# Optimization experiments

Measured on AMD Instinct MI355X. Metric: run time of the kernel, lower is better.

## Reference

```python
import jax, jax.numpy as jnp
import numpy as np

B, L, D = 4, 4096, 1024
S, H, DH = 256, 16, 64
TOPK = 8
NEG_INF = float('-inf')


def setup_inputs() -> dict:
    key = jax.random.key(0)
    ks = jax.random.split(key, 10)
    scale = 1.0 / np.sqrt(D)
    return {
        'token_states': jax.random.normal(ks[0], (B, L, D), dtype=jnp.float32),
        'Z_sets': jax.random.normal(ks[1], (B, S, H, DH), dtype=jnp.float32),
        'desc_q': jax.random.normal(ks[2], (B, S, D), dtype=jnp.float32),
        'mask_q': jnp.ones((B, S), dtype=bool),
        'Wg_w': jax.random.normal(ks[3], (D, D), dtype=jnp.float32) * scale,
        'Wg_b': jnp.zeros((D,), dtype=jnp.float32),
        'Wd_w': jax.random.normal(ks[4], (D, D), dtype=jnp.float32) * scale,
        'Wd_b': jnp.zeros((D,), dtype=jnp.float32),
        'out_w': jax.random.normal(ks[5], (D, D), dtype=jnp.float32) * scale,
        'out_b': jnp.zeros((D,), dtype=jnp.float32),
    }


def reference(token_states, Z_sets, desc_q, mask_q, Wg_w, Wg_b, Wd_w, Wd_b, out_w, out_b):
    # torch nn.Linear: y = x @ W.T + b
    Tproj = token_states @ Wg_w.T + Wg_b          # (B,L,D)
    Dproj = desc_q @ Wd_w.T + Wd_b                # (B,S,D)
    logits = jnp.einsum('bld,bsd->bls', Tproj, Dproj)  # (B,L,S)
    logits = jnp.where(mask_q[:, None, :], logits, NEG_INF)
    if TOPK > 0 and S > TOPK:
        vals, idx = jax.lax.top_k(logits, TOPK)   # (B,L,K)
        probs = jax.nn.softmax(vals, axis=-1)     # softmax over the K kept logits
        b_ix = jnp.arange(B)[:, None, None]
        l_ix = jnp.arange(L)[None, :, None]
        G = jnp.zeros_like(logits).at[b_ix, l_ix, idx].set(probs)
    else:
        G = jax.nn.softmax(logits, axis=-1)
    mix = jnp.einsum('bls,bshd->blhd', G, Z_sets)  # (B,L,H,DH)
    return mix.reshape(B, L, D) @ out_w.T + out_b
```

## Files before the change

### kernel.cpp

```cpp
#include <hip/hip_runtime.h>
#include <hip/hip_bf16.h>
#include <stdint.h>


#define B_ 4
#define L_ 4096
#define D_ 1024
#define S_ 256

typedef short s16x8 __attribute__((ext_vector_type(8)));
typedef float f32x4 __attribute__((ext_vector_type(4)));

__device__ __forceinline__ unsigned short f2bf(float f) {
  uint32_t u = __float_as_uint(f);
  u += 0x7FFFu + ((u >> 16) & 1u);
  return (unsigned short)(u >> 16);
}
__device__ __forceinline__ float bf2f(unsigned short h) {
  return __uint_as_float(((uint32_t)h) << 16);
}
__device__ __forceinline__ int kperm32(int k5) {
  return (((k5 >> 2) & 3) << 3) | (((k5 >> 4) & 1) << 2) | (k5 & 3);
}

__global__ __launch_bounds__(256)
void prep_all(const float* __restrict__ desc, const float* __restrict__ Zf,
              const float* __restrict__ Wd, const float* __restrict__ oW,
              const float* __restrict__ Wg,
              unsigned short* __restrict__ dHi, unsigned short* __restrict__ dLo,
              unsigned short* __restrict__ zHi,
              unsigned short* __restrict__ wdHi, unsigned short* __restrict__ wdLo,
              unsigned short* __restrict__ owHi,
              unsigned short* __restrict__ wgTHi, unsigned short* __restrict__ wgTLo) {
  __shared__ float t[64][65];
  const int bid = blockIdx.x, tid = threadIdx.x;
  if (bid < 4096) {
    const float* src[4] = {desc, Zf, Wd, oW};
    unsigned short* hi[4] = {dHi, zHi, wdHi, owHi};
    unsigned short* lo[4] = {dLo, nullptr, wdLo, nullptr};
    int job = bid >> 10;
    int i = (bid & 1023) * 256 + tid;
    float4 v = reinterpret_cast<const float4*>(src[job])[i];
    int idx = i << 2;
    int nidx = (idx & ~31) | (((idx >> 2) & 3) << 3) | (((idx >> 4) & 1) << 2);
    float a[4] = {v.x, v.y, v.z, v.w};
    unsigned short hb[4];
#pragma unroll
    for (int e = 0; e < 4; ++e) hb[e] = f2bf(a[e]);
    *reinterpret_cast<ushort4*>(hi[job] + nidx) = make_ushort4(hb[0], hb[1], hb[2], hb[3]);
    if (lo[job]) {
      unsigned short lb[4];
#pragma unroll
      for (int e = 0; e < 4; ++e) lb[e] = f2bf(a[e] - bf2f(hb[e]));
      *reinterpret_cast<ushort4*>(lo[job] + nidx) = make_ushort4(lb[0], lb[1], lb[2], lb[3]);
    }
  } else {
    int tb = bid - 4096;
    int bx = tb & 15, by = tb >> 4;
    int c = tid & 63, r0 = tid >> 6;
#pragma unroll
    for (int rr = 0; rr < 16; ++rr) {
      int r = r0 * 16 + rr;
      t[r][c] = Wg[(size_t)(by * 64 + r) * 1024 + bx * 64 + c];
    }
    __syncthreads();
#pragma unroll
    for (int rr = 0; rr < 16; ++rr) {
      int r = r0 * 16 + rr;
      float v = t[c][r];
      int kcol = by * 64 + (c & 32) + kperm32(c & 31);
      size_t o = (size_t)(bx * 64 + r) * 1024 + kcol;
      unsigned short hb = f2bf(v);
      wgTHi[o] = hb;
      wgTLo[o] = f2bf(v - bf2f(hb));
    }
  }
}

__global__ __launch_bounds__(256, 2)
void gemm_a(const unsigned short* __restrict__ dHi, const unsigned short* __restrict__ dLo,
            const unsigned short* __restrict__ wdHi, const unsigned short* __restrict__ wdLo,
            const unsigned short* __restrict__ zHi, const unsigned short* __restrict__ owHi,
            float* __restrict__ P) {
  __shared__ unsigned short lAh[128 * 64], lAl[128 * 64];
  __shared__ unsigned short lBh[128 * 64], lBl[128 * 64];
  const int tid = threadIdx.x;
  const int w = tid >> 6, l = tid & 63;
  const int g = l >> 4, r15 = l & 15;
  const int rowBase = blockIdx.y * 128, colBase = blockIdx.x * 128;
  const int prob = blockIdx.z >> 1, kz = blockIdx.z & 1;
  const bool t3 = (prob == 0);
  const unsigned short* Ah = t3 ? dHi : zHi;
  const unsigned short* Bh = t3 ? wdHi : owHi;
  const int wr = (w >> 1) * 64, wc = (w & 1) * 64;
  const int k0 = kz * 512;

  f32x4 acc[4][4] = {};

  for (int kt = k0; kt < k0 + 512; kt += 64) {
    __syncthreads();
#pragma unroll
    for (int j = 0; j < 4; ++j) {
      int cl = j * 256 + tid;
      int r = cl >> 3;
      int c16 = (cl & 7) ^ (r & 7);
      long ao = (long)(rowBase + r) * 1024 + kt + c16 * 8;
      long bo = (long)(colBase + r) * 1024 + kt + c16 * 8;
      size_t doff = (size_t)(j * 256 + w * 64) * 8;
      __builtin_amdgcn_global_load_lds((const __attribute__((address_space(1))) void*)(Ah + ao),
                                       (__attribute__((address_space(3))) void*)(lAh + doff), 16, 0, 0);
      __builtin_amdgcn_global_load_lds((const __attribute__((address_space(1))) void*)(Bh + bo),
                                       (__attribute__((address_space(3))) void*)(lBh + doff), 16, 0, 0);
      if (t3) {
        __builtin_amdgcn_global_load_lds((const __attribute__((address_space(1))) void*)(dLo + ao),
                                         (__attribute__((address_space(3))) void*)(lAl + doff), 16, 0, 0);
        __builtin_amdgcn_global_load_lds((const __attribute__((address_space(1))) void*)(wdLo + bo),
                                         (__attribute__((address_space(3))) void*)(lBl + doff), 16, 0, 0);
      }
    }
    __syncthreads();
#pragma unroll
    for (int ks = 0; ks < 2; ++ks) {
      s16x8 ah[4], bh[4];
#pragma unroll
      for (int m = 0; m < 4; ++m) {
        int row = wr + m * 16 + r15;
        int offb = (row * 128 + ks * 64 + g * 16) ^ ((row & 7) << 4);
        ah[m] = *reinterpret_cast<const s16x8*>(reinterpret_cast<const char*>(lAh) + offb);
      }
#pragma unroll
      for (int n = 0; n < 4; ++n) {
        int row = wc + n * 16 + r15;
        int offb = (row * 128 + ks * 64 + g * 16) ^ ((row & 7) << 4);
        bh[n] = *reinterpret_cast<const s16x8*>(reinterpret_cast<const char*>(lBh) + offb);
      }
#pragma unroll
      for (int m = 0; m < 4; ++m)
#pragma unroll
        for (int n = 0; n < 4; ++n)
          acc[m][n] = __builtin_amdgcn_mfma_f32_16x16x32_bf16(ah[m], bh[n], acc[m][n], 0, 0, 0);
      if (t3) {
        s16x8 al[4], bl[4];
#pragma unroll
        for (int m = 0; m < 4; ++m) {
          int row = wr + m * 16 + r15;
          int offb = (row * 128 + ks * 64 + g * 16) ^ ((row & 7) << 4);
          al[m] = *reinterpret_cast<const s16x8*>(reinterpret_cast<const char*>(lAl) + offb);
        }
#pragma unroll
        for (int n = 0; n < 4; ++n) {
          int row = wc + n * 16 + r15;
          int offb = (row * 128 + ks * 64 + g * 16) ^ ((row & 7) << 4);
          bl[n] = *reinterpret_cast<const s16x8*>(reinterpret_cast<const char*>(lBl) + offb);
        }
#pragma unroll
        for (int m = 0; m < 4; ++m)
#pragma unroll
          for (int n = 0; n < 4; ++n) {
            acc[m][n] = __builtin_amdgcn_mfma_f32_16x16x32_bf16(al[m], bh[n], acc[m][n], 0, 0, 0);
            acc[m][n] = __builtin_amdgcn_mfma_f32_16x16x32_bf16(ah[m], bl[n], acc[m][n], 0, 0, 0);
          }
      }
    }
  }

  float* Cz = P + (long)blockIdx.z * (1 << 20);
#pragma unroll
  for (int m = 0; m < 4; ++m)
#pragma unroll
    for (int n = 0; n < 4; ++n) {
      int col = colBase + wc + n * 16 + r15;
#pragma unroll
      for (int q = 0; q < 4; ++q) {
        int row = rowBase + wr + m * 16 + g * 4 + q;
        Cz[(long)row * 1024 + col] = acc[m][n][q];
      }
    }
}

template <int KSPLIT>
__global__ __launch_bounds__(256, 2)
void gemm_f3(const unsigned short* __restrict__ Ahi, const unsigned short* __restrict__ Alo,
             const unsigned short* __restrict__ Bhi, const unsigned short* __restrict__ Blo,
             float* __restrict__ C, int K, long partStride) {
  __shared__ unsigned short lAh[128 * 64], lAl[128 * 64];
  __shared__ unsigned short lBh[128 * 64], lBl[128 * 64];
  const int tid = threadIdx.x;
  const int w = tid >> 6, l = tid & 63;
  const int g = l >> 4, r15 = l & 15;
  const int rowBase = blockIdx.y * 128, colBase = blockIdx.x * 128;
  const int kz = blockIdx.z % KSPLIT;
  const int wr = (w >> 1) * 64, wc = (w & 1) * 64;
  const int chunk = K / KSPLIT, k0 = kz * chunk;

  f32x4 acc[4][4] = {};

  for (int kt = k0; kt < k0 + chunk; kt += 64) {
    __syncthreads();
#pragma unroll
    for (int j = 0; j < 4; ++j) {
      int cl = j * 256 + tid;
      int r = cl >> 3;
      int c16 = (cl & 7) ^ (r & 7);
      long ao = (long)(rowBase + r) * K + kt + c16 * 8;
      long bo = (long)(colBase + r) * K + kt + c16 * 8;
      size_t doff = (size_t)(j * 256 + w * 64) * 8;
      __builtin_amdgcn_global_load_lds((const __attribute__((address_space(1))) void*)(Ahi + ao),
                                       (__attribute__((address_space(3))) void*)(lAh + doff), 16, 0, 0);
      __builtin_amdgcn_global_load_lds((const __attribute__((address_space(1))) void*)(Alo + ao),
                                       (__attribute__((address_space(3))) void*)(lAl + doff), 16, 0, 0);
      __builtin_amdgcn_global_load_lds((const __attribute__((address_space(1))) void*)(Bhi + bo),
                                       (__attribute__((address_space(3))) void*)(lBh + doff), 16, 0, 0);
      __builtin_amdgcn_global_load_lds((const __attribute__((address_space(1))) void*)(Blo + bo),
                                       (__attribute__((address_space(3))) void*)(lBl + doff), 16, 0, 0);
    }
    __syncthreads();
#pragma unroll
    for (int ks = 0; ks < 2; ++ks) {
      s16x8 ah[4], al[4], bh[4], bl[4];
#pragma unroll
      for (int m = 0; m < 4; ++m) {
        int row = wr + m * 16 + r15;
        int offb = (row * 128 + ks * 64 + g * 16) ^ ((row & 7) << 4);
        ah[m] = *reinterpret_cast<const s16x8*>(reinterpret_cast<const char*>(lAh) + offb);
        al[m] = *reinterpret_cast<const s16x8*>(reinterpret_cast<const char*>(lAl) + offb);
      }
#pragma unroll
      for (int n = 0; n < 4; ++n) {
        int row = wc + n * 16 + r15;
        int offb = (row * 128 + ks * 64 + g * 16) ^ ((row & 7) << 4);
        bh[n] = *reinterpret_cast<const s16x8*>(reinterpret_cast<const char*>(lBh) + offb);
        bl[n] = *reinterpret_cast<const s16x8*>(reinterpret_cast<const char*>(lBl) + offb);
      }
#pragma unroll
      for (int m = 0; m < 4; ++m)
#pragma unroll
        for (int n = 0; n < 4; ++n) {
          acc[m][n] = __builtin_amdgcn_mfma_f32_16x16x32_bf16(ah[m], bh[n], acc[m][n], 0, 0, 0);
          acc[m][n] = __builtin_amdgcn_mfma_f32_16x16x32_bf16(al[m], bh[n], acc[m][n], 0, 0, 0);
          acc[m][n] = __builtin_amdgcn_mfma_f32_16x16x32_bf16(ah[m], bl[n], acc[m][n], 0, 0, 0);
        }
    }
  }

  float* Cz = C + (long)blockIdx.z * partStride;
#pragma unroll
  for (int m = 0; m < 4; ++m)
#pragma unroll
    for (int n = 0; n < 4; ++n) {
      int col = colBase + wc + n * 16 + r15;
#pragma unroll
      for (int q = 0; q < 4; ++q) {
        int row = rowBase + wr + m * 16 + g * 4 + q;
        Cz[(long)row * 1024 + col] = acc[m][n][q];
      }
    }
}

__global__ __launch_bounds__(256)
void post_a(const float* __restrict__ P, const float* __restrict__ Wd_b,
            const float* __restrict__ out_b, const float* __restrict__ Wg_b,
            unsigned short* __restrict__ dpHi, unsigned short* __restrict__ dpLo,
            unsigned short* __restrict__ zwB, float* __restrict__ cb) {
  int w = threadIdx.x >> 6, l = threadIdx.x & 63;
  int job = blockIdx.x;
  if (job < 256) {
    int row = job * 4 + w;
    const float* r0 = P + (size_t)row * 1024;
    const float* r1 = r0 + (1 << 20);
    float s = 0.f;
#pragma unroll
    for (int j = 0; j < 4; ++j) {
      int i = j * 64 + l;
      float4 a = reinterpret_cast<const float4*>(r0)[i];
      float4 b = reinterpret_cast<const float4*>(r1)[i];
      float4 bb = reinterpret_cast<const float4*>(Wd_b)[i & 255];
      float4 v = make_float4(a.x + b.x + bb.x, a.y + b.y + bb.y,
                             a.z + b.z + bb.z, a.w + b.w + bb.w);
      float4 g = reinterpret_cast<const float4*>(Wg_b)[i & 255];
      s += v.x * g.x + v.y * g.y + v.z * g.z + v.w * g.w;
      int idx = i << 2;
      int nidx = (idx & ~31) | (((idx >> 2) & 3) << 3) | (((idx >> 4) & 1) << 2);
      float arr[4] = {v.x, v.y, v.z, v.w};
      unsigned short hb[4], lb[4];
#pragma unroll
      for (int e = 0; e < 4; ++e) {
        hb[e] = f2bf(arr[e]);
        lb[e] = f2bf(arr[e] - bf2f(hb[e]));
      }
      *reinterpret_cast<ushort4*>(dpHi + (size_t)row * 1024 + nidx) =
          make_ushort4(hb[0], hb[1], hb[2], hb[3]);
      *reinterpret_cast<ushort4*>(dpLo + (size_t)row * 1024 + nidx) =
          make_ushort4(lb[0], lb[1], lb[2], lb[3]);
    }
#pragma unroll
    for (int off = 32; off; off >>= 1) s += __shfl_xor(s, off);
    if (l == 0) cb[row] = s;
  } else {
    int row = (job - 256) * 4 + w;
    const float* r0 = P + 2 * (1 << 20) + (size_t)row * 1024;
    const float* r1 = r0 + (1 << 20);
#pragma unroll
    for (int j = 0; j < 4; ++j) {
      int i = j * 64 + l;
      float4 a = reinterpret_cast<const float4*>(r0)[i];
      float4 b = reinterpret_cast<const float4*>(r1)[i];
      float4 bb = reinterpret_cast<const float4*>(out_b)[i & 255];
      *reinterpret_cast<ushort4*>(zwB + (size_t)row * 1024 + (i << 2)) =
          make_ushort4(f2bf(a.x + b.x + bb.x), f2bf(a.y + b.y + bb.y),
                       f2bf(a.z + b.z + bb.z), f2bf(a.w + b.w + bb.w));
    }
  }
}

__global__ __launch_bounds__(256)
void post_mt(const float* __restrict__ P, unsigned short* __restrict__ hi,
             unsigned short* __restrict__ lo) {
  int w = threadIdx.x >> 6, l = threadIdx.x & 63;
  int row = blockIdx.x * 4 + w;
  const float* r0 = P + (size_t)row * 1024;
#pragma unroll
  for (int j = 0; j < 4; ++j) {
    int i = j * 64 + l;
    float4 a = reinterpret_cast<const float4*>(r0)[i];
    float4 b = reinterpret_cast<const float4*>(r0 + (1 << 20))[i];
    float4 c = reinterpret_cast<const float4*>(r0 + 2 * (1 << 20))[i];
    float4 d = reinterpret_cast<const float4*>(r0 + 3 * (1 << 20))[i];
    float arr[4] = {a.x + b.x + c.x + d.x, a.y + b.y + c.y + d.y,
                    a.z + b.z + c.z + d.z, a.w + b.w + c.w + d.w};
    int idx = i << 2;
    int nidx = (idx & ~31) | (((idx >> 2) & 3) << 3) | (((idx >> 4) & 1) << 2);
    unsigned short hb[4], lb[4];
#pragma unroll
    for (int e = 0; e < 4; ++e) {
      hb[e] = f2bf(arr[e]);
      lb[e] = f2bf(arr[e] - bf2f(hb[e]));
    }
    *reinterpret_cast<ushort4*>(hi + (size_t)row * 1024 + nidx) =
        make_ushort4(hb[0], hb[1], hb[2], hb[3]);
    *reinterpret_cast<ushort4*>(lo + (size_t)row * 1024 + nidx) =
        make_ushort4(lb[0], lb[1], lb[2], lb[3]);
  }
}

template <int KSPLIT>
__global__ __launch_bounds__(256, 2)
void gemm_af32(const float* __restrict__ A,
               const unsigned short* __restrict__ Bhi, const unsigned short* __restrict__ Blo,
               float* __restrict__ Ct, int K,
               long batchA, long batchB, long batchCt, long kzStrideCt) {
  __shared__ unsigned short lAh[128 * 64], lAl[128 * 64];
  __shared__ unsigned short lBh[128 * 64], lBl[128 * 64];
  const int tid = threadIdx.x;
  const int w = tid >> 6, l = tid & 63;
  const int g = l >> 4, r15 = l & 15;
  const int nwg = gridDim.x * gridDim.y * gridDim.z;
  int h = blockIdx.x + gridDim.x * (blockIdx.y + gridDim.y * blockIdx.z);
  int lg = (h % 8) * (nwg / 8) + h / 8;
  const int bx = lg % gridDim.x;
  const int by = (lg / gridDim.x) % gridDim.y;
  const int bzz = lg / (gridDim.x * gridDim.y);
  const int rowBase = by * 128, colBase = bx * 128;
  const int bz = bzz / KSPLIT, kz = bzz % KSPLIT;
  const long zA = (long)bz * batchA, zB = (long)bz * batchB;
  const int wr = (w >> 1) * 64, wc = (w & 1) * 64;
  const int chunk = K / KSPLIT, k0 = kz * chunk;

  f32x4 acc[4][4] = {};

  for (int kt = k0; kt < k0 + chunk; kt += 64) {
    float4 av[8];
#pragma unroll
    for (int j = 0; j < 8; ++j) {
      int cl = j * 256 + tid;
      int r = cl >> 4, k4 = cl & 15;
      av[j] = *reinterpret_cast<const float4*>(A + zA + (long)(rowBase + r) * K + kt + k4 * 4);
    }
    __syncthreads();
#pragma unroll
    for (int j = 0; j < 4; ++j) {
      int cl = j * 256 + tid;
      int r = cl >> 3;
      int c16 = (cl & 7) ^ (r & 7);
      long bo = zB + (long)(colBase + r) * K + kt + c16 * 8;
      size_t doff = (size_t)(j * 256 + w * 64) * 8;
      __builtin_amdgcn_global_load_lds((const __attribute__((address_space(1))) void*)(Bhi + bo),
                                       (__attribute__((address_space(3))) void*)(lBh + doff), 16, 0, 0);
      __builtin_amdgcn_global_load_lds((const __attribute__((address_space(1))) void*)(Blo + bo),
                                       (__attribute__((address_space(3))) void*)(lBl + doff), 16, 0, 0);
    }
#pragma unroll
    for (int j = 0; j < 8; ++j) {
      int cl = j * 256 + tid;
      int r = cl >> 4, k4 = cl & 15;
      int byteoff = r * 128 + ((k4 >> 3) << 6) + ((k4 & 3) << 4) + (((k4 >> 2) & 1) << 3);
      int swz = byteoff ^ ((r & 7) << 4);
      uint32_t u0 = __float_as_uint(av[j].x), u1 = __float_as_uint(av[j].y);
      uint32_t u2 = __float_as_uint(av[j].z), u3 = __float_as_uint(av[j].w);
      float r0f = av[j].x - __uint_as_float(u0 & 0xFFFF0000u);
      float r1f = av[j].y - __uint_as_float(u1 & 0xFFFF0000u);
      float r2f = av[j].z - __uint_as_float(u2 & 0xFFFF0000u);
      float r3f = av[j].w - __uint_as_float(u3 & 0xFFFF0000u);
      *reinterpret_cast<ushort4*>(reinterpret_cast<char*>(lAh) + swz) =
          make_ushort4((unsigned short)(u0 >> 16), (unsigned short)(u1 >> 16),
                       (unsigned short)(u2 >> 16), (unsigned short)(u3 >> 16));
      *reinterpret_cast<ushort4*>(reinterpret_cast<char*>(lAl) + swz) =
          make_ushort4((unsigned short)(__float_as_uint(r0f) >> 16),
                       (unsigned short)(__float_as_uint(r1f) >> 16),
                       (unsigned short)(__float_as_uint(r2f) >> 16),
                       (unsigned short)(__float_as_uint(r3f) >> 16));
    }
    __syncthreads();
#pragma unroll
    for (int ks = 0; ks < 2; ++ks) {
      s16x8 ah[4], al[4], bh[4], bl[4];
#pragma unroll
      for (int m = 0; m < 4; ++m) {
        int row = wr + m * 16 + r15;
        int offb = (row * 128 + ks * 64 + g * 16) ^ ((row & 7) << 4);
        ah[m] = *reinterpret_cast<const s16x8*>(reinterpret_cast<const char*>(lAh) + offb);
        al[m] = *reinterpret_cast<const s16x8*>(reinterpret_cast<const char*>(lAl) + offb);
      }
#pragma unroll
      for (int n = 0; n < 4; ++n) {
        int row = wc + n * 16 + r15;
        int offb = (row * 128 + ks * 64 + g * 16) ^ ((row & 7) << 4);
        bh[n] = *reinterpret_cast<const s16x8*>(reinterpret_cast<const char*>(lBh) + offb);
        bl[n] = *reinterpret_cast<const s16x8*>(reinterpret_cast<const char*>(lBl) + offb);
      }
#pragma unroll
      for (int m = 0; m < 4; ++m)
#pragma unroll
        for (int n = 0; n < 4; ++n) {
          acc[m][n] = __builtin_amdgcn_mfma_f32_16x16x32_bf16(ah[m], bh[n], acc[m][n], 0, 0, 0);
          acc[m][n] = __builtin_amdgcn_mfma_f32_16x16x32_bf16(al[m], bh[n], acc[m][n], 0, 0, 0);
          acc[m][n] = __builtin_amdgcn_mfma_f32_16x16x32_bf16(ah[m], bl[n], acc[m][n], 0, 0, 0);
        }
    }
  }

  float* Cz = Ct + kz * kzStrideCt + (long)bz * batchCt;
#pragma unroll
  for (int m = 0; m < 4; ++m)
#pragma unroll
    for (int n = 0; n < 4; ++n) {
      int col = colBase + wc + n * 16 + r15;
      int row0 = rowBase + wr + m * 16 + g * 4;
      *reinterpret_cast<float4*>(Cz + (long)col * L_ + row0) =
          make_float4(acc[m][n][0], acc[m][n][1], acc[m][n][2], acc[m][n][3]);
    }
}

__global__ __launch_bounds__(64)
void topk8_k(const float* __restrict__ lt, const float* __restrict__ cb,
             int* __restrict__ tokIdx, float* __restrict__ tokP) {
  int t = blockIdx.x * 64 + threadIdx.x;
  int b = t >> 12, l = t & 4095;
  const float* p0 = lt + (long)b * (256 * 4096) + l;
  const float* p1 = p0 + (1 << 22);
  const float* cbb = cb + b * 256;
  uint32_t v0 = 0, v1 = 0, v2 = 0, v3 = 0, v4 = 0, v5 = 0, v6 = 0, v7 = 0;
  auto loadb = [&](float* dst, int s0) {
#pragma unroll
    for (int u = 0; u < 8; ++u) {
      long o = (long)(s0 + u) * 4096;
      dst[u] = p0[o] + p1[o] + cbb[s0 + u];
    }
  };
  auto insert = [&](const float* val, int s0) {
#pragma unroll
    for (int u = 0; u < 8; ++u) {
      uint32_t iu = __float_as_uint(val[u]);
      uint32_t x = (iu ^ ((uint32_t)((int)iu >> 31) | 0x80000000u));
      x = (x & 0xFFFFFF00u) | (uint32_t)(255 - (s0 + u));
      uint32_t w0 = (x > v1) ? v1 : (x > v0 ? x : v0);
      uint32_t w1 = (x > v2) ? v2 : (x > v1 ? x : v1);
      uint32_t w2 = (x > v3) ? v3 : (x > v2 ? x : v2);
      uint32_t w3 = (x > v4) ? v4 : (x > v3 ? x : v3);
      uint32_t w4 = (x > v5) ? v5 : (x > v4 ? x : v4);
      uint32_t w5 = (x > v6) ? v6 : (x > v5 ? x : v5);
      uint32_t w6 = (x > v7) ? v7 : (x > v6 ? x : v6);
      uint32_t w7 = (x > v7) ? x : v7;
      v0 = w0; v1 = w1; v2 = w2; v3 = w3; v4 = w4; v5 = w5; v6 = w6; v7 = w7;
    }
  };
  float va[8], vb[8];
  loadb(va, 0);
  for (int s0 = 0; s0 < 256; s0 += 16) {
    loadb(vb, s0 + 8);
    insert(va, s0);
    if (s0 + 16 < 256) loadb(va, s0 + 16);
    insert(vb, s0 + 8);
  }
  uint32_t keys[8] = {v0, v1, v2, v3, v4, v5, v6, v7};
  float vals[8];
  int sidx[8];
#pragma unroll
  for (int i = 0; i < 8; ++i) {
    int s = 255 - (int)(keys[i] & 255u);
    sidx[i] = s;
    long o = (long)s * 4096;
    vals[i] = p0[o] + p1[o] + cbb[s];
  }
  float m = vals[0];
#pragma unroll
  for (int i = 1; i < 8; ++i) m = fmaxf(m, vals[i]);
  float p[8], ssum = 0.f;
#pragma unroll
  for (int i = 0; i < 8; ++i) { p[i] = __expf(vals[i] - m); ssum += p[i]; }
  float inv = 1.f / ssum;
#pragma unroll
  for (int i = 0; i < 8; ++i) {
    tokIdx[(long)t * 8 + i] = b * 256 + sidx[i];
    tokP[(long)t * 8 + i] = p[i] * inv;
  }
}

__global__ __launch_bounds__(256)
void mix_k(const int* __restrict__ tokIdx, const float* __restrict__ tokP,
           const unsigned short* __restrict__ zwB, float* __restrict__ out) {
  int w = threadIdx.x >> 6, l = threadIdx.x & 63;
  long t = (long)blockIdx.x * 4 + w;
  int ridx[8];
  float wt[8];
#pragma unroll
  for (int i = 0; i < 8; ++i) {
    ridx[i] = tokIdx[t * 8 + i];
    wt[i] = tokP[t * 8 + i];
  }
  float acc[16] = {};
#pragma unroll
  for (int i = 0; i < 8; ++i) {
    const unsigned short* zr = zwB + (long)ridx[i] * 1024 + l * 16;
    uint4 q0 = *reinterpret_cast<const uint4*>(zr);
    uint4 q1 = *reinterpret_cast<const uint4*>(zr + 8);
    uint32_t qs[8] = {q0.x, q0.y, q0.z, q0.w, q1.x, q1.y, q1.z, q1.w};
#pragma unroll
    for (int e = 0; e < 8; ++e) {
      acc[e * 2]     += wt[i] * __uint_as_float(qs[e] << 16);
      acc[e * 2 + 1] += wt[i] * __uint_as_float(qs[e] & 0xFFFF0000u);
    }
  }
  float* orow = out + t * 1024 + l * 16;
#pragma unroll
  for (int j = 0; j < 4; ++j)
    reinterpret_cast<float4*>(orow)[j] =
        make_float4(acc[j * 4], acc[j * 4 + 1], acc[j * 4 + 2], acc[j * 4 + 3]);
}

extern "C" void kernel_launch(void* const* d_in, const int* in_sizes, int n_in,
                              void* d_out, int out_size, void* d_ws, size_t ws_size,
                              hipStream_t stream) {
  const float* token = (const float*)d_in[0];
  const float* Z     = (const float*)d_in[1];
  const float* descq = (const float*)d_in[2];
  const float* Wg    = (const float*)d_in[4];
  const float* Wg_b  = (const float*)d_in[5];
  const float* Wd    = (const float*)d_in[6];
  const float* Wd_b  = (const float*)d_in[7];
  const float* outW  = (const float*)d_in[8];
  const float* out_b = (const float*)d_in[9];
  float* out = (float*)d_out;
  (void)in_sizes; (void)n_in; (void)out_size; (void)ws_size;

  char* ws = (char*)d_ws;
  const size_t MB = 1u << 20;
  unsigned short* dHi   = (unsigned short*)(ws + 0 * MB);
  unsigned short* dLo   = (unsigned short*)(ws + 2 * MB);
  unsigned short* wdHi  = (unsigned short*)(ws + 4 * MB);
  unsigned short* wdLo  = (unsigned short*)(ws + 6 * MB);
  unsigned short* zHi   = (unsigned short*)(ws + 8 * MB);
  unsigned short* owHi  = (unsigned short*)(ws + 10 * MB);
  unsigned short* wgTHi = (unsigned short*)(ws + 12 * MB);
  unsigned short* wgTLo = (unsigned short*)(ws + 14 * MB);
  float*          P     = (float*)         (ws + 16 * MB);
  unsigned short* dpHi  = (unsigned short*)(ws + 32 * MB);
  unsigned short* dpLo  = (unsigned short*)(ws + 34 * MB);
  unsigned short* zwB   = (unsigned short*)(ws + 36 * MB);
  unsigned short* mtHi  = (unsigned short*)(ws + 38 * MB);
  unsigned short* mtLo  = (unsigned short*)(ws + 40 * MB);
  int*            tokIdx= (int*)           (ws + 42 * MB);
  float*          tokP  = (float*)         (ws + 42 * MB + 512 * 1024);
  float*          cb    = (float*)         (ws + 43 * MB);
  float*          lt    = (float*)         (ws + 0 * MB);

  prep_all<<<4352, 256, 0, stream>>>(descq, Z, Wd, outW, Wg,
                                     dHi, dLo, zHi, wdHi, wdLo, owHi,
                                     wgTHi, wgTLo);

  gemm_a<<<dim3(8, 8, 4), 256, 0, stream>>>(dHi, dLo, wdHi, wdLo, zHi, owHi, P);

  post_a<<<512, 256, 0, stream>>>(P, Wd_b, out_b, Wg_b, dpHi, dpLo, zwB, cb);

  gemm_f3<4><<<dim3(8, 8, 4), 256, 0, stream>>>(dpHi, dpLo, wgTHi, wgTLo, P,
                                                1024, 1048576L);

  post_mt<<<256, 256, 0, stream>>>(P, mtHi, mtLo);

  gemm_af32<2><<<dim3(2, 32, 8), 256, 0, stream>>>(token, mtHi, mtLo, lt, 1024,
                                                   (long)L_ * D_, (long)S_ * D_,
                                                   (long)L_ * S_, 4194304L);

  topk8_k<<<256, 64, 0, stream>>>(lt, cb, tokIdx, tokP);

  mix_k<<<4096, 256, 0, stream>>>(tokIdx, tokP, zwB, out);
}
```

Baseline: 139.3 us.

## Enlarge token GEMM tile to 256x128 with 512-thread blocks

Reworks the token-by-M^T GEMM so each 512-thread workgroup computes a 256x128 tile, with 8 waves sharing one B tile in LDS. Batch, K-split and tile indices are now hardcoded, and the grid-order swizzle is remapped to match. The goal is to halve B-tile reloads from global memory and raise per-block reuse. In exchange, LDS grows to 96KB per block and only one block fits per CU, which lowers occupancy and latency hiding.

```diff
diff --git a/kernel.cpp b/kernel.cpp
--- a/kernel.cpp
+++ b/kernel.cpp
@@ -343,47 +343,47 @@
   }
 }
 
-template <int KSPLIT>
-__global__ __launch_bounds__(256, 2)
+__global__ __launch_bounds__(512, 1)
 void gemm_af32(const float* __restrict__ A,
                const unsigned short* __restrict__ Bhi, const unsigned short* __restrict__ Blo,
-               float* __restrict__ Ct, int K,
-               long batchA, long batchB, long batchCt, long kzStrideCt) {
-  __shared__ unsigned short lAh[128 * 64], lAl[128 * 64];
+               float* __restrict__ Ct, long kzStrideCt) {
+  __shared__ unsigned short lAh[256 * 64], lAl[256 * 64];
   __shared__ unsigned short lBh[128 * 64], lBl[128 * 64];
   const int tid = threadIdx.x;
-  const int w = tid >> 6, l = tid & 63;
+  const int wid = tid >> 6, l = tid & 63;
   const int g = l >> 4, r15 = l & 15;
-  const int nwg = gridDim.x * gridDim.y * gridDim.z;
-  int h = blockIdx.x + gridDim.x * (blockIdx.y + gridDim.y * blockIdx.z);
-  int lg = (h % 8) * (nwg / 8) + h / 8;
-  const int bx = lg % gridDim.x;
-  const int by = (lg / gridDim.x) % gridDim.y;
-  const int bzz = lg / (gridDim.x * gridDim.y);
-  const int rowBase = by * 128, colBase = bx * 128;
-  const int bz = bzz / KSPLIT, kz = bzz % KSPLIT;
-  const long zA = (long)bz * batchA, zB = (long)bz * batchB;
-  const int wr = (w >> 1) * 64, wc = (w & 1) * 64;
-  const int chunk = K / KSPLIT, k0 = kz * chunk;
+  int h = blockIdx.x + 2 * (blockIdx.y + 64 * blockIdx.z);
+  int lg = (h & 7) * 32 + (h >> 3);
+  const int bx = lg & 1;
+  const int by = (lg >> 1) & 63;
+  const int kz = lg >> 7;
+  const int batch = by >> 4;
+  const int rowBase = (by & 15) * 256;
+  const int colBase = bx * 128;
+  const long zA = (long)batch * (L_ * D_);
+  const long zB = (long)batch * (S_ * D_);
+  const int wr = (wid >> 1) * 64;
+  const int wc = (wid & 1) * 64;
+  const int k0 = kz * 512;
 
   f32x4 acc[4][4] = {};
 
-  for (int kt = k0; kt < k0 + chunk; kt += 64) {
+  for (int kt = k0; kt < k0 + 512; kt += 64) {
     float4 av[8];
 #pragma unroll
     for (int j = 0; j < 8; ++j) {
-      int cl = j * 256 + tid;
+      int cl = j * 512 + tid;
       int r = cl >> 4, k4 = cl & 15;
-      av[j] = *reinterpret_cast<const float4*>(A + zA + (long)(rowBase + r) * K + kt + k4 * 4);
+      av[j] = *reinterpret_cast<const float4*>(A + zA + (long)(rowBase + r) * 1024 + kt + k4 * 4);
     }
     __syncthreads();
 #pragma unroll
-    for (int j = 0; j < 4; ++j) {
-      int cl = j * 256 + tid;
+    for (int j = 0; j < 2; ++j) {
+      int cl = j * 512 + tid;
       int r = cl >> 3;
       int c16 = (cl & 7) ^ (r & 7);
-      long bo = zB + (long)(colBase + r) * K + kt + c16 * 8;
-      size_t doff = (size_t)(j * 256 + w * 64) * 8;
+      long bo = zB + (long)(colBase + r) * 1024 + kt + c16 * 8;
+      size_t doff = (size_t)(j * 512 + wid * 64) * 8;
       __builtin_amdgcn_global_load_lds((const __attribute__((address_space(1))) void*)(Bhi + bo),
                                        (__attribute__((address_space(3))) void*)(lBh + doff), 16, 0, 0);
       __builtin_amdgcn_global_load_lds((const __attribute__((address_space(1))) void*)(Blo + bo),
@@ -391,7 +391,7 @@
     }
 #pragma unroll
     for (int j = 0; j < 8; ++j) {
-      int cl = j * 256 + tid;
+      int cl = j * 512 + tid;
       int r = cl >> 4, k4 = cl & 15;
       int byteoff = r * 128 + ((k4 >> 3) << 6) + ((k4 & 3) << 4) + (((k4 >> 2) & 1) << 3);
       int swz = byteoff ^ ((r & 7) << 4);
@@ -439,7 +439,7 @@
     }
   }
 
-  float* Cz = Ct + kz * kzStrideCt + (long)bz * batchCt;
+  float* Cz = Ct + kz * kzStrideCt + (long)batch * ((long)L_ * S_);
 #pragma unroll
   for (int m = 0; m < 4; ++m)
 #pragma unroll
@@ -597,9 +597,7 @@
 
   post_mt<<<256, 256, 0, stream>>>(P, mtHi, mtLo);
 
-  gemm_af32<2><<<dim3(2, 32, 8), 256, 0, stream>>>(token, mtHi, mtLo, lt, 1024,
-                                                   (long)L_ * D_, (long)S_ * D_,
-                                                   (long)L_ * S_, 4194304L);
+  gemm_af32<<<dim3(2, 64, 2), 512, 0, stream>>>(token, mtHi, mtLo, lt, 4194304L);
 
   topk8_k<<<256, 64, 0, stream>>>(lt, cb, tokIdx, tokP);
 
```

New measurement: 145.3 us. 1.04x slower.

## Use single-bf16 logits GEMM and refine top-8 logits in fp32 inside mix

Applied to the files above, without the earlier changes.

The token-by-descriptor logits GEMM drops its split-precision (hi/lo) bf16 scheme and uses one bf16 MFMA per tile instead of three. This cuts MFMA work, LDS traffic and the lo-operand loads. To recover accuracy, the top-k kernel now emits raw approximate logits, and the mix kernel recomputes each selected logit exactly in fp32 from the token row and an fp32 copy of the fused matrix before the softmax. The risk is that the top-8 selection itself may differ from the reference when approximate logits are near-tied, and the mix kernel gains extra token and matrix reads.

```diff
diff --git a/kernel.cpp b/kernel.cpp
--- a/kernel.cpp
+++ b/kernel.cpp
@@ -315,7 +315,7 @@
 
 __global__ __launch_bounds__(256)
 void post_mt(const float* __restrict__ P, unsigned short* __restrict__ hi,
-             unsigned short* __restrict__ lo) {
+             float* __restrict__ mtF) {
   int w = threadIdx.x >> 6, l = threadIdx.x & 63;
   int row = blockIdx.x * 4 + w;
   const float* r0 = P + (size_t)row * 1024;
@@ -328,29 +328,26 @@
     float4 d = reinterpret_cast<const float4*>(r0 + 3 * (1 << 20))[i];
     float arr[4] = {a.x + b.x + c.x + d.x, a.y + b.y + c.y + d.y,
                     a.z + b.z + c.z + d.z, a.w + b.w + c.w + d.w};
+    *reinterpret_cast<float4*>(mtF + (size_t)row * 1024 + (i << 2)) =
+        make_float4(arr[0], arr[1], arr[2], arr[3]);
     int idx = i << 2;
     int nidx = (idx & ~31) | (((idx >> 2) & 3) << 3) | (((idx >> 4) & 1) << 2);
-    unsigned short hb[4], lb[4];
-#pragma unroll
-    for (int e = 0; e < 4; ++e) {
-      hb[e] = f2bf(arr[e]);
-      lb[e] = f2bf(arr[e] - bf2f(hb[e]));
-    }
+    unsigned short hb[4];
+#pragma unroll
+    for (int e = 0; e < 4; ++e) hb[e] = f2bf(arr[e]);
     *reinterpret_cast<ushort4*>(hi + (size_t)row * 1024 + nidx) =
         make_ushort4(hb[0], hb[1], hb[2], hb[3]);
-    *reinterpret_cast<ushort4*>(lo + (size_t)row * 1024 + nidx) =
-        make_ushort4(lb[0], lb[1], lb[2], lb[3]);
   }
 }
 
 template <int KSPLIT>
 __global__ __launch_bounds__(256, 2)
 void gemm_af32(const float* __restrict__ A,
-               const unsigned short* __restrict__ Bhi, const unsigned short* __restrict__ Blo,
+               const unsigned short* __restrict__ Bhi,
                float* __restrict__ Ct, int K,
                long batchA, long batchB, long batchCt, long kzStrideCt) {
-  __shared__ unsigned short lAh[128 * 64], lAl[128 * 64];
-  __shared__ unsigned short lBh[128 * 64], lBl[128 * 64];
+  __shared__ unsigned short lAh[128 * 64];
+  __shared__ unsigned short lBh[128 * 64];
   const int tid = threadIdx.x;
   const int w = tid >> 6, l = tid & 63;
   const int g = l >> 4, r15 = l & 15;
@@ -386,8 +383,6 @@
       size_t doff = (size_t)(j * 256 + w * 64) * 8;
       __builtin_amdgcn_global_load_lds((const __attribute__((address_space(1))) void*)(Bhi + bo),
                                        (__attribute__((address_space(3))) void*)(lBh + doff), 16, 0, 0);
-      __builtin_amdgcn_global_load_lds((const __attribute__((address_space(1))) void*)(Blo + bo),
-                                       (__attribute__((address_space(3))) void*)(lBl + doff), 16, 0, 0);
     }
 #pragma unroll
     for (int j = 0; j < 8; ++j) {
@@ -395,47 +390,33 @@
       int r = cl >> 4, k4 = cl & 15;
       int byteoff = r * 128 + ((k4 >> 3) << 6) + ((k4 & 3) << 4) + (((k4 >> 2) & 1) << 3);
       int swz = byteoff ^ ((r & 7) << 4);
-      uint32_t u0 = __float_as_uint(av[j].x), u1 = __float_as_uint(av[j].y);
-      uint32_t u2 = __float_as_uint(av[j].z), u3 = __float_as_uint(av[j].w);
-      float r0f = av[j].x - __uint_as_float(u0 & 0xFFFF0000u);
-      float r1f = av[j].y - __uint_as_float(u1 & 0xFFFF0000u);
-      float r2f = av[j].z - __uint_as_float(u2 & 0xFFFF0000u);
-      float r3f = av[j].w - __uint_as_float(u3 & 0xFFFF0000u);
       *reinterpret_cast<ushort4*>(reinterpret_cast<char*>(lAh) + swz) =
-          make_ushort4((unsigned short)(u0 >> 16), (unsigned short)(u1 >> 16),
-                       (unsigned short)(u2 >> 16), (unsigned short)(u3 >> 16));
-      *reinterpret_cast<ushort4*>(reinterpret_cast<char*>(lAl) + swz) =
-          make_ushort4((unsigned short)(__float_as_uint(r0f) >> 16),
-                       (unsigned short)(__float_as_uint(r1f) >> 16),
-                       (unsigned short)(__float_as_uint(r2f) >> 16),
-                       (unsigned short)(__float_as_uint(r3f) >> 16));
+          make_ushort4((unsigned short)(__float_as_uint(av[j].x) >> 16),
+                       (unsigned short)(__float_as_uint(av[j].y) >> 16),
+                       (unsigned short)(__float_as_uint(av[j].z) >> 16),
+                       (unsigned short)(__float_as_uint(av[j].w) >> 16));
     }
     __syncthreads();
 #pragma unroll
     for (int ks = 0; ks < 2; ++ks) {
-      s16x8 ah[4], al[4], bh[4], bl[4];
+      s16x8 ah[4], bh[4];
 #pragma unroll
       for (int m = 0; m < 4; ++m) {
         int row = wr + m * 16 + r15;
         int offb = (row * 128 + ks * 64 + g * 16) ^ ((row & 7) << 4);
         ah[m] = *reinterpret_cast<const s16x8*>(reinterpret_cast<const char*>(lAh) + offb);
-        al[m] = *reinterpret_cast<const s16x8*>(reinterpret_cast<const char*>(lAl) + offb);
       }
 #pragma unroll
       for (int n = 0; n < 4; ++n) {
         int row = wc + n * 16 + r15;
         int offb = (row * 128 + ks * 64 + g * 16) ^ ((row & 7) << 4);
         bh[n] = *reinterpret_cast<const s16x8*>(reinterpret_cast<const char*>(lBh) + offb);
-        bl[n] = *reinterpret_cast<const s16x8*>(reinterpret_cast<const char*>(lBl) + offb);
       }
 #pragma unroll
       for (int m = 0; m < 4; ++m)
 #pragma unroll
-        for (int n = 0; n < 4; ++n) {
+        for (int n = 0; n < 4; ++n)
           acc[m][n] = __builtin_amdgcn_mfma_f32_16x16x32_bf16(ah[m], bh[n], acc[m][n], 0, 0, 0);
-          acc[m][n] = __builtin_amdgcn_mfma_f32_16x16x32_bf16(al[m], bh[n], acc[m][n], 0, 0, 0);
-          acc[m][n] = __builtin_amdgcn_mfma_f32_16x16x32_bf16(ah[m], bl[n], acc[m][n], 0, 0, 0);
-        }
     }
   }
 
@@ -453,7 +434,7 @@
 
 __global__ __launch_bounds__(64)
 void topk8_k(const float* __restrict__ lt, const float* __restrict__ cb,
-             int* __restrict__ tokIdx, float* __restrict__ tokP) {
+             int* __restrict__ tokIdx, float* __restrict__ tokAv) {
   int t = blockIdx.x * 64 + threadIdx.x;
   int b = t >> 12, l = t & 4095;
   const float* p0 = lt + (long)b * (256 * 4096) + l;
@@ -493,52 +474,73 @@
     insert(vb, s0 + 8);
   }
   uint32_t keys[8] = {v0, v1, v2, v3, v4, v5, v6, v7};
-  float vals[8];
-  int sidx[8];
 #pragma unroll
   for (int i = 0; i < 8; ++i) {
     int s = 255 - (int)(keys[i] & 255u);
-    sidx[i] = s;
     long o = (long)s * 4096;
-    vals[i] = p0[o] + p1[o] + cbb[s];
-  }
-  float m = vals[0];
-#pragma unroll
-  for (int i = 1; i < 8; ++i) m = fmaxf(m, vals[i]);
-  float p[8], ssum = 0.f;
-#pragma unroll
-  for (int i = 0; i < 8; ++i) { p[i] = __expf(vals[i] - m); ssum += p[i]; }
-  float inv = 1.f / ssum;
-#pragma unroll
-  for (int i = 0; i < 8; ++i) {
-    tokIdx[(long)t * 8 + i] = b * 256 + sidx[i];
-    tokP[(long)t * 8 + i] = p[i] * inv;
+    tokIdx[(long)t * 8 + i] = b * 256 + s;
+    tokAv[(long)t * 8 + i] = p0[o] + p1[o] + cbb[s];
   }
 }
 
 __global__ __launch_bounds__(256)
-void mix_k(const int* __restrict__ tokIdx, const float* __restrict__ tokP,
-           const unsigned short* __restrict__ zwB, float* __restrict__ out) {
+void refine_mix_k(const int* __restrict__ tokIdx, const float* __restrict__ tokAv,
+                  const float* __restrict__ token, const float* __restrict__ mtF,
+                  const float* __restrict__ cb, const unsigned short* __restrict__ zwB,
+                  float* __restrict__ out) {
   int w = threadIdx.x >> 6, l = threadIdx.x & 63;
   long t = (long)blockIdx.x * 4 + w;
-  int ridx[8];
-  float wt[8];
+  int sidx[8];
+  float av[8];
 #pragma unroll
   for (int i = 0; i < 8; ++i) {
-    ridx[i] = tokIdx[t * 8 + i];
-    wt[i] = tokP[t * 8 + i];
-  }
+    sidx[i] = tokIdx[t * 8 + i];
+    av[i] = tokAv[t * 8 + i];
+  }
+  const float* trow = token + t * 1024 + l * 16;
+  float4 tok[4];
+#pragma unroll
+  for (int j = 0; j < 4; ++j) tok[j] = reinterpret_cast<const float4*>(trow)[j];
+  float amax = av[0];
+#pragma unroll
+  for (int i = 1; i < 8; ++i) amax = fmaxf(amax, av[i]);
+  float vals[8];
+#pragma unroll
+  for (int i = 0; i < 8; ++i) {
+    if (av[i] >= amax - 16.f) {
+      const float* mrow = mtF + (long)sidx[i] * 1024 + l * 16;
+      float p = 0.f;
+#pragma unroll
+      for (int j = 0; j < 4; ++j) {
+        float4 m4 = reinterpret_cast<const float4*>(mrow)[j];
+        p += tok[j].x * m4.x + tok[j].y * m4.y + tok[j].z * m4.z + tok[j].w * m4.w;
+      }
+#pragma unroll
+      for (int off = 32; off; off >>= 1) p += __shfl_xor(p, off);
+      vals[i] = p + cb[sidx[i]];
+    } else {
+      vals[i] = av[i];
+    }
+  }
+  float m = vals[0];
+#pragma unroll
+  for (int i = 1; i < 8; ++i) m = fmaxf(m, vals[i]);
+  float p8[8], ssum = 0.f;
+#pragma unroll
+  for (int i = 0; i < 8; ++i) { p8[i] = __expf(vals[i] - m); ssum += p8[i]; }
+  float inv = 1.f / ssum;
   float acc[16] = {};
 #pragma unroll
   for (int i = 0; i < 8; ++i) {
-    const unsigned short* zr = zwB + (long)ridx[i] * 1024 + l * 16;
+    float wt = p8[i] * inv;
+    const unsigned short* zr = zwB + (long)sidx[i] * 1024 + l * 16;
     uint4 q0 = *reinterpret_cast<const uint4*>(zr);
     uint4 q1 = *reinterpret_cast<const uint4*>(zr + 8);
     uint32_t qs[8] = {q0.x, q0.y, q0.z, q0.w, q1.x, q1.y, q1.z, q1.w};
 #pragma unroll
     for (int e = 0; e < 8; ++e) {
-      acc[e * 2]     += wt[i] * __uint_as_float(qs[e] << 16);
-      acc[e * 2 + 1] += wt[i] * __uint_as_float(qs[e] & 0xFFFF0000u);
+      acc[e * 2]     += wt * __uint_as_float(qs[e] << 16);
+      acc[e * 2 + 1] += wt * __uint_as_float(qs[e] & 0xFFFF0000u);
     }
   }
   float* orow = out + t * 1024 + l * 16;
@@ -578,10 +580,10 @@
   unsigned short* dpLo  = (unsigned short*)(ws + 34 * MB);
   unsigned short* zwB   = (unsigned short*)(ws + 36 * MB);
   unsigned short* mtHi  = (unsigned short*)(ws + 38 * MB);
-  unsigned short* mtLo  = (unsigned short*)(ws + 40 * MB);
-  int*            tokIdx= (int*)           (ws + 42 * MB);
-  float*          tokP  = (float*)         (ws + 42 * MB + 512 * 1024);
-  float*          cb    = (float*)         (ws + 43 * MB);
+  float*          mtF   = (float*)         (ws + 40 * MB);
+  int*            tokIdx= (int*)           (ws + 44 * MB);
+  float*          tokAv = (float*)         (ws + 44 * MB + 512 * 1024);
+  float*          cb    = (float*)         (ws + 45 * MB);
   float*          lt    = (float*)         (ws + 0 * MB);
 
   prep_all<<<4352, 256, 0, stream>>>(descq, Z, Wd, outW, Wg,
@@ -595,13 +597,13 @@
   gemm_f3<4><<<dim3(8, 8, 4), 256, 0, stream>>>(dpHi, dpLo, wgTHi, wgTLo, P,
                                                 1024, 1048576L);
 
-  post_mt<<<256, 256, 0, stream>>>(P, mtHi, mtLo);
-
-  gemm_af32<2><<<dim3(2, 32, 8), 256, 0, stream>>>(token, mtHi, mtLo, lt, 1024,
+  post_mt<<<256, 256, 0, stream>>>(P, mtHi, mtF);
+
+  gemm_af32<2><<<dim3(2, 32, 8), 256, 0, stream>>>(token, mtHi, lt, 1024,
                                                    (long)L_ * D_, (long)S_ * D_,
                                                    (long)L_ * S_, 4194304L);
 
-  topk8_k<<<256, 64, 0, stream>>>(lt, cb, tokIdx, tokP);
-
-  mix_k<<<4096, 256, 0, stream>>>(tokIdx, tokP, zwB, out);
-}
+  topk8_k<<<256, 64, 0, stream>>>(lt, cb, tokIdx, tokAv);
+
+  refine_mix_k<<<4096, 256, 0, stream>>>(tokIdx, tokAv, token, mtF, cb, zwB, out);
+}
```

Result: slower. 151.2 us (+8.5%).
